# Kernel optimization log

Measured on AMD Instinct MI355X. Metric: run time of the kernel, lower is better.

## Reference

```python
import jax, jax.numpy as jnp
import numpy as np

N = 200000   # nodes (Elliptic-scale)
E = 500000   # directed edges
F = 166      # in_channels / node feature dim
H = 128      # hidden_channels
C = 2        # out_channels
T = 49       # number of time steps


def setup_inputs() -> dict:
    key = jax.random.key(0)
    ks = jax.random.split(key, 12)
    x = jax.random.normal(ks[0], (N, F), jnp.float32)
    edge_index = jax.random.randint(ks[1], (2, E), 0, N, dtype=jnp.int32)
    time_step = jax.random.randint(ks[2], (N,), 0, T, dtype=jnp.int32)
    sF = 1.0 / np.sqrt(F)
    sH = 1.0 / np.sqrt(H)
    initial_w = jax.random.uniform(ks[3], (F, F), jnp.float32, -sF, sF)
    gru_w_ih = jax.random.uniform(ks[4], (3 * F, F), jnp.float32, -sF, sF)
    gru_w_hh = jax.random.uniform(ks[5], (3 * F, F), jnp.float32, -sF, sF)
    gru_b_ih = jax.random.uniform(ks[6], (3 * F,), jnp.float32, -sF, sF)
    gru_b_hh = jax.random.uniform(ks[7], (3 * F,), jnp.float32, -sF, sF)
    proj_w = jax.random.uniform(ks[8], (H, F), jnp.float32, -sF, sF)
    proj_b = jax.random.uniform(ks[9], (H,), jnp.float32, -sF, sF)
    cls_w = jax.random.uniform(ks[10], (C, H), jnp.float32, -sH, sH)
    cls_b = jax.random.uniform(ks[11], (C,), jnp.float32, -sH, sH)
    return {"x": x, "edge_index": edge_index, "time_step": time_step,
            "initial_w": initial_w, "gru_w_ih": gru_w_ih, "gru_w_hh": gru_w_hh,
            "gru_b_ih": gru_b_ih, "gru_b_hh": gru_b_hh,
            "proj_w": proj_w, "proj_b": proj_b, "cls_w": cls_w, "cls_b": cls_b}


def reference(x, edge_index, time_step, initial_w, gru_w_ih, gru_w_hh,
              gru_b_ih, gru_b_hh, proj_w, proj_b, cls_w, cls_b):
    src, dst = edge_index[0], edge_index[1]
    n = x.shape[0]

    def gru(W):
        # torch.nn.GRU single step, input = hidden = W  (FxF matrix, rows = batch)
        gi = W @ gru_w_ih.T + gru_b_ih
        gh = W @ gru_w_hh.T + gru_b_hh
        i_r, i_z, i_n = jnp.split(gi, 3, axis=-1)
        h_r, h_z, h_n = jnp.split(gh, 3, axis=-1)
        r = jax.nn.sigmoid(i_r + h_r)
        z = jax.nn.sigmoid(i_z + h_z)
        nn_ = jnp.tanh(i_n + r * h_n)
        return (1.0 - z) * nn_ + z * W

    def step(carry, t):
        W, logits = carry
        W = gru(W)  # evolve GCN weight (EvolveGCN-O)
        # subgraph of nodes with time_step <= t, expressed by masking (same math
        # as relabel+extract: inactive nodes contribute nothing, their outputs are ignored)
        act = time_step <= t
        ew = (act[src] & act[dst]).astype(x.dtype)
        # gcn_norm with self-loops: deg = in-degree over active edges + 1
        deg = jax.ops.segment_sum(ew, dst, num_segments=n) + 1.0
        dinv = jax.lax.rsqrt(deg)
        norm = ew * dinv[src] * dinv[dst]
        h = jnp.where(act[:, None], x, 0.0) @ W               # [N, F]
        agg = jax.ops.segment_sum(h[src] * norm[:, None], dst, num_segments=n)
        agg = agg + h / deg[:, None]                          # self-loop term dinv_i^2 * h_i
        z = jax.nn.relu(agg @ proj_w.T + proj_b)              # [N, H] (dropout: eval mode)
        lg = z @ cls_w.T + cls_b                              # [N, C]
        logits = jnp.where((time_step == t)[:, None], lg, logits)
        return (W, logits), None

    init = (initial_w, jnp.zeros((n, cls_w.shape[0]), x.dtype))
    (_, logits), _ = jax.lax.scan(step, init, jnp.arange(T, dtype=time_step.dtype))
    return logits
```

## Files before the change

kernel.cpp:

```cpp
#include <hip/hip_runtime.h>
#include <hip/hip_fp16.h>
#include <math.h>

#define NN 200000
#define NE 500000
#define FF 166
#define HH 128
#define CC 2
#define TT 49
#define GG 498
#define PADN 203136
#define MAXTILES 6400
#define KP 84
#define KPAD 192
#define SCB 512
#define SNB 391
#define HB 782
#define CIB 1954
#define XSB 37500
#define P2B 210
#define C2B 977
#define H2B 391
#define DEGB 782
#define MBB (TT * 96)

typedef _Float16 half2v __attribute__((ext_vector_type(2)));
typedef _Float16 f16x4 __attribute__((ext_vector_type(4)));
typedef _Float16 f16x8 __attribute__((ext_vector_type(8)));
typedef float f32x4 __attribute__((ext_vector_type(4)));

static __device__ __forceinline__ float fdot2f(half2v a, half2v b, float c) {
#if __has_builtin(__builtin_amdgcn_fdot2)
    return __builtin_amdgcn_fdot2(a, b, c, false);
#else
    return c + (float)a.x * (float)b.x + (float)a.y * (float)b.y;
#endif
}

__global__ __launch_bounds__(512) void setup1(
        const float* __restrict__ wih, const float* __restrict__ whh,
        const float* __restrict__ projw,
        _Float16* __restrict__ wkp, float* __restrict__ projwT,
        const int* __restrict__ dstp, int* __restrict__ offc,
        const int* __restrict__ ts, int* __restrict__ cnt, int* __restrict__ rank) {
    __shared__ int h2[2][TT];
    int b = blockIdx.x;
    int tid = threadIdx.x;
    if (b < P2B) {
        int idx = b * 512 + tid;
        const int A = 2 * KP * 512;
        if (idx < A) {
            int m = idx / (KP * 512);
            int r = idx - m * (KP * 512);
            int kp = r >> 9, c = r & 511;
            const float* Wm = m ? whh : wih;
            float x0 = 0.0f, x1 = 0.0f;
            if (c < GG) {
                int k0 = 2 * kp, k1 = 2 * kp + 1;
                if (k0 < FF) x0 = Wm[c * FF + k0];
                if (k1 < FF) x1 = Wm[c * FF + k1];
            }
            wkp[2 * idx]     = (_Float16)x0;
            wkp[2 * idx + 1] = (_Float16)x1;
        } else if (idx < A + FF * HH) {
            int q = idx - A;
            int k = q >> 7, hh = q & 127;
            projwT[q] = projw[hh * FF + k];
        }
    } else if (b < P2B + C2B) {
        int e = (b - P2B) * 512 + tid;
        if (e < NE) atomicAdd(&offc[dstp[e]], 1);
    } else {
        int hb2 = b - P2B - C2B;
        int sub = tid >> 8;
        int lt = tid & 255;
        if (lt < TT) h2[sub][lt] = 0;
        __syncthreads();
        int i = hb2 * 512 + tid;
        if (i < NN) {
            int t = ts[i];
            rank[i] = atomicAdd(&h2[sub][t], 1);
        }
        __syncthreads();
        if (lt < TT) cnt[(hb2 * 2 + sub) * TT + lt] = h2[sub][lt];
    }
}

__global__ __launch_bounds__(512) void gru_evolve(
        const float* __restrict__ initial_w,
        const _Float16* __restrict__ wkp,
        const float* __restrict__ bih, const float* __restrict__ bhh,
        float* __restrict__ W_all) {
    __shared__ float s_w[FF];
    __shared__ __align__(16) _Float16 s_wh[2 * KP];
    __shared__ float s_pre[2][512];
    int tid = threadIdx.x;
    int row = blockIdx.x;

    if (tid < FF) {
        float v = initial_w[(size_t)row * FF + tid];
        s_w[tid] = v;
        s_wh[tid] = (_Float16)v;
    } else if (tid < 2 * KP) {
        s_wh[tid] = (_Float16)0.0f;
    }

    int cc0 = tid * 2;
    bool act = cc0 < 996;
    int m = (cc0 >= 498) ? 1 : 0;
    int c0 = act ? (cc0 - m * 498) : 0;

    half2v wr0[KP], wr1[KP];
    {
        const half2v* __restrict__ pW =
            (const half2v*)wkp + (size_t)(act ? m : 0) * (KP * 512) + c0;
        #pragma unroll
        for (int kp = 0; kp < KP; ++kp) {
            wr0[kp] = pW[(size_t)(kp << 9)];
            wr1[kp] = pW[(size_t)(kp << 9) + 1];
        }
    }

    float bi_r = 0, bi_z = 0, bi_n = 0, bh_r = 0, bh_z = 0, bh_n = 0;
    if (tid < FF) {
        bi_r = bih[tid]; bi_z = bih[FF + tid]; bi_n = bih[2 * FF + tid];
        bh_r = bhh[tid]; bh_z = bhh[FF + tid]; bh_n = bhh[2 * FF + tid];
    }
    __syncthreads();

    const f16x8* s_wh8 = (const f16x8*)s_wh;
    for (int t = 0; t < TT; ++t) {
        if (act) {
            float a0 = 0.0f, a1 = 0.0f;
            #pragma unroll
            for (int q = 0; q < 21; ++q) {
                f16x8 w8 = s_wh8[q];
                half2v h0 = __builtin_shufflevector(w8, w8, 0, 1);
                half2v h1 = __builtin_shufflevector(w8, w8, 2, 3);
                half2v h2 = __builtin_shufflevector(w8, w8, 4, 5);
                half2v h3 = __builtin_shufflevector(w8, w8, 6, 7);
                a0 = fdot2f(wr0[4 * q + 0], h0, a0);  a1 = fdot2f(wr1[4 * q + 0], h0, a1);
                a0 = fdot2f(wr0[4 * q + 1], h1, a0);  a1 = fdot2f(wr1[4 * q + 1], h1, a1);
                a0 = fdot2f(wr0[4 * q + 2], h2, a0);  a1 = fdot2f(wr1[4 * q + 2], h2, a1);
                a0 = fdot2f(wr0[4 * q + 3], h3, a0);  a1 = fdot2f(wr1[4 * q + 3], h3, a1);
            }
            s_pre[m][c0]     = a0;
            s_pre[m][c0 + 1] = a1;
        }
        __syncthreads();
        if (tid < FF) {
            float i_r = s_pre[0][tid]          + bi_r;
            float h_r = s_pre[1][tid]          + bh_r;
            float i_z = s_pre[0][FF + tid]     + bi_z;
            float h_z = s_pre[1][FF + tid]     + bh_z;
            float i_n = s_pre[0][2 * FF + tid] + bi_n;
            float h_n = s_pre[1][2 * FF + tid] + bh_n;
            float rg = 1.0f / (1.0f + expf(-(i_r + h_r)));
            float zg = 1.0f / (1.0f + expf(-(i_z + h_z)));
            float ng = tanhf(i_n + rg * h_n);
            float wnew = (1.0f - zg) * ng + zg * s_w[tid];
            s_w[tid] = wnew;
            s_wh[tid] = (_Float16)wnew;
            W_all[((size_t)t * FF + row) * FF + tid] = wnew;
        }
        __syncthreads();
    }
}

__global__ __launch_bounds__(256) void setup2(
        const int* __restrict__ off, int* __restrict__ bsum,
        const int* __restrict__ cnt, int* __restrict__ basecol, int* __restrict__ bcnt) {
    __shared__ int s[256];
    int b = blockIdx.x, tid = threadIdx.x;
    if (b < SNB) {
        int i0 = b * SCB + tid * 2;
        int v = 0;
        if (i0 < NN) v += off[i0];
        if (i0 + 1 < NN) v += off[i0 + 1];
        s[tid] = v;
        __syncthreads();
        for (int d = 128; d > 0; d >>= 1) {
            if (tid < d) s[tid] += s[tid + d];
            __syncthreads();
        }
        if (tid == 0) bsum[b] = s[0];
    } else {
        int t = b - SNB;
        const int CH = (HB + 255) / 256;
        int b0 = tid * CH;
        int loc[4];
        int sum = 0;
        for (int u = 0; u < CH; ++u) {
            int bb = b0 + u;
            int v = (bb < HB) ? cnt[bb * TT + t] : 0;
            loc[u] = sum;
            sum += v;
        }
        s[tid] = sum;
        __syncthreads();
        for (int d = 1; d < 256; d <<= 1) {
            int u = (tid >= d) ? s[tid - d] : 0;
            __syncthreads();
            s[tid] += u;
            __syncthreads();
        }
        int base = s[tid] - sum;
        for (int u = 0; u < CH; ++u) {
            int bb = b0 + u;
            if (bb < HB) basecol[bb * TT + t] = base + loc[u];
        }
        if (tid == 255) bcnt[t] = s[255];
    }
}

__global__ __launch_bounds__(512) void setup3(
        const int* __restrict__ bsum, int* __restrict__ bpre, int* __restrict__ off,
        const int* __restrict__ bcnt, int* __restrict__ pstart,
        int* __restrict__ tile_t, int* __restrict__ tile_r0, int* __restrict__ meta) {
    __shared__ int s[512];
    int tid = threadIdx.x;
    if (blockIdx.x == 0) {
        int v = (tid < SNB) ? bsum[tid] : 0;
        s[tid] = v;
        __syncthreads();
        for (int d = 1; d < 512; d <<= 1) {
            int u = (tid >= d) ? s[tid - d] : 0;
            __syncthreads();
            s[tid] += u;
            __syncthreads();
        }
        bpre[tid] = s[tid] - v;
        if (tid == 511) off[NN] = s[511];
    } else {
        int t = tid;
        int nt = (t < TT) ? (bcnt[t] + 31) / 32 : 0;
        if (t < 64) s[t] = nt;
        __syncthreads();
        for (int d = 1; d < 64; d <<= 1) {
            int v = (t >= d && t < 64) ? s[t - d] : 0;
            __syncthreads();
            if (t < 64) s[t] += v;
            __syncthreads();
        }
        if (t < 64) {
            int ntbase = s[t] - nt;
            int pbase = ntbase * 32;
            if (t < TT) {
                pstart[t] = pbase;
                for (int u = 0; u < nt; ++u) {
                    tile_t[ntbase + u] = t;
                    tile_r0[ntbase + u] = pbase + u * 32;
                }
            }
            if (t == 63) {
                meta[0] = s[63];
                meta[1] = s[63] * 32;
                pstart[TT] = s[63] * 32;
            }
        }
    }
}

__global__ __launch_bounds__(512) void setup4(
        int* __restrict__ off, const int* __restrict__ bpre,
        const int* __restrict__ ts, const int* __restrict__ rank,
        const int* __restrict__ basecol, const int* __restrict__ pstart,
        int* __restrict__ perm, int* __restrict__ pos) {
    __shared__ int s[512];
    int b = blockIdx.x, tid = threadIdx.x;
    if (b < SNB) {
        int i = b * SCB + tid;
        int v = (i < NN) ? off[i] : 0;
        s[tid] = v;
        __syncthreads();
        for (int d = 1; d < 512; d <<= 1) {
            int u = (tid >= d) ? s[tid - d] : 0;
            __syncthreads();
            s[tid] += u;
            __syncthreads();
        }
        if (i < NN) off[i] = s[tid] - v + bpre[b];
    } else {
        int i = (b - SNB) * 512 + tid;
        if (i < NN) {
            int t = ts[i];
            int hb = i >> 8;
            int p = pstart[t] + basecol[hb * TT + t] + rank[i];
            perm[p] = i;
            pos[i] = p;
        }
    }
}

__global__ __launch_bounds__(256) void setup5(
        const int* __restrict__ srcp, const int* __restrict__ dstp,
        const int* __restrict__ ts, const int* __restrict__ off,
        int* __restrict__ cursor, int2* __restrict__ adjst,
        const float* __restrict__ x, const int* __restrict__ pos,
        f16x4* __restrict__ x2p4) {
    int b = blockIdx.x, tid = threadIdx.x;
    if (b < CIB) {
        int e = b * 256 + tid;
        if (e < NE) {
            int d = dstp[e];
            int s2 = srcp[e];
            int p = atomicAdd(&cursor[d], 1);
            adjst[off[d] + p] = make_int2(s2, (ts[s2] << 25) | pos[s2]);
        }
    } else {
        int idx = (b - CIB) * 256 + tid;
        if (idx >= NN * 48) return;
        int i = idx / 48, cp4 = idx - i * 48;
        int c0 = cp4 * 4;
        float v0 = 0.f, v1 = 0.f, v2 = 0.f, v3 = 0.f;
        const float* xr = x + (size_t)i * FF;
        if (c0 + 3 < FF) {
            float2 p0 = *(const float2*)(xr + c0);
            float2 p1 = *(const float2*)(xr + c0 + 2);
            v0 = p0.x; v1 = p0.y; v2 = p1.x; v3 = p1.y;
        } else if (c0 < FF) {
            float2 p0 = *(const float2*)(xr + c0);
            v0 = p0.x; v1 = p0.y;
        }
        f16x4 h;
        h[0] = (_Float16)v0; h[1] = (_Float16)v1;
        h[2] = (_Float16)v2; h[3] = (_Float16)v3;
        x2p4[(size_t)pos[i] * 48 + cp4] = h;
    }
}

__global__ __launch_bounds__(256) void degf_m(
        const int* __restrict__ off, const int2* __restrict__ adjst,
        const int* __restrict__ ts, _Float16* __restrict__ dinvh,
        float* __restrict__ selfdeg,
        const float* __restrict__ W_all, const float* __restrict__ projwT,
        _Float16* __restrict__ Mh) {
    __shared__ unsigned short sh[TT * 256];
    __shared__ __align__(16) float sw2[2][168];
    int b = blockIdx.x;
    int tid = threadIdx.x;
    if (b < DEGB) {
        int i = b * 256 + tid;
        for (int t = 0; t < TT; ++t) sh[t * 256 + tid] = 0;
        if (i >= NN) return;
        int tsi = ts[i];
        int e0 = off[i], e1 = off[i + 1];
        for (int e = e0; e < e1; ++e) {
            int tj = adjst[e].y >> 25;
            sh[tj * 256 + tid]++;
        }
        int cum = 1;
        for (int t = 0; t < TT; ++t) {
            cum += sh[t * 256 + tid];
            dinvh[(size_t)t * NN + i] = (_Float16)rsqrtf((float)cum);
            if (t == tsi) selfdeg[i] = 1.0f / (float)cum;
        }
    } else {
        int mb = b - DEGB;
        int t = mb / 96, rb = mb - t * 96;
        int r0 = rb * 2;
        for (int idx = tid; idx < 2 * FF; idx += 256) {
            int rr = idx / FF, k = idx - rr * FF;
            int r = r0 + rr;
            sw2[rr][k] = (r < FF) ? W_all[((size_t)t * FF + r) * FF + k] : 0.0f;
        }
        __syncthreads();
        int rr = tid >> 7, h = tid & 127;
        int r = r0 + rr;
        float acc = 0.0f;
        if (r < FF) {
            const float* __restrict__ pw = projwT + h;
            #pragma unroll 4
            for (int c4 = 0; c4 < 164; c4 += 4) {
                float4 w = *(const float4*)&sw2[rr][c4];
                acc += w.x * pw[(size_t)(c4 + 0) << 7];
                acc += w.y * pw[(size_t)(c4 + 1) << 7];
                acc += w.z * pw[(size_t)(c4 + 2) << 7];
                acc += w.w * pw[(size_t)(c4 + 3) << 7];
            }
            acc += sw2[rr][164] * pw[(size_t)164 << 7];
            acc += sw2[rr][165] * pw[(size_t)165 << 7];
        }
        Mh[((size_t)t * HH + h) * KPAD + r] = (_Float16)acc;
    }
}

__global__ __launch_bounds__(256) void edge_compact(
        const int* __restrict__ off, const int2* __restrict__ adjst,
        const int* __restrict__ ts, const _Float16* __restrict__ dinvh,
        int2* __restrict__ ewp, int* __restrict__ nact) {
    int i = blockIdx.x * 256 + threadIdx.x;
    if (i >= NN) return;
    int t = ts[i];
    const _Float16* dv = dinvh + (size_t)t * NN;
    float dvi = (float)dv[i];
    int e0 = off[i], e1 = off[i + 1];
    int c = e0;
    for (int e = e0; e < e1; ++e) {
        int2 a = adjst[e];
        if ((a.y >> 25) <= t) {
            float w = (float)dv[a.x] * dvi;
            ewp[c++] = make_int2(a.y & 0x1FFFFFF, __float_as_int(w));
        }
    }
    nact[i] = c - e0;
}

__global__ __launch_bounds__(512) void gemm_fused5(
        const int* __restrict__ meta, const int* __restrict__ tile_t,
        const int* __restrict__ tile_r0, const int* __restrict__ perm,
        const float* __restrict__ selfdeg, const f16x4* __restrict__ x2p4,
        const int* __restrict__ off, const int* __restrict__ nact,
        const int2* __restrict__ ewp,
        const _Float16* __restrict__ Mh, const float* __restrict__ proj_b,
        const float* __restrict__ cls_w, const float* __restrict__ cls_b,
        float* __restrict__ out) {
    __shared__ __align__(16) char smraw[32 * 130 * 4];
    _Float16* sY = (_Float16*)smraw;
    float* sP = (float*)smraw;
    int bid = blockIdx.x;
    if (bid >= meta[0]) return;
    int t = tile_t[bid], r0 = tile_r0[bid];
    int tid = threadIdx.x;
    int lane = tid & 63;
    int w = tid >> 6;
    bool ln48 = lane < 48;

    {
        const uint4* src = (const uint4*)(x2p4 + (size_t)r0 * 48);
        #pragma unroll
        for (int u = 0; u < 2; ++u) {
            int q = tid + u * 512;
            if (q < 768) {
                int row = q / 24, kc = q - row * 24;
                *(uint4*)(sY + row * 200 + kc * 8) = src[q];
            }
        }
    }
    __syncthreads();

    int rbase = w * 4;
    int ep[4], ee[4];
    float ac[4][4];
    #pragma unroll
    for (int q = 0; q < 4; ++q) {
        int r = rbase + q;
        int i = perm[r0 + r];
        float sw = 0.0f;
        ep[q] = 0; ee[q] = 0;
        if (i >= 0) {
            sw = selfdeg[i];
            ep[q] = off[i];
            ee[q] = ep[q] + nact[i];
        }
        f16x4 h = (f16x4)((_Float16)0.0f);
        if (ln48) h = *(const f16x4*)(sY + r * 200 + lane * 4);
        ac[q][0] = sw * (float)h[0];
        ac[q][1] = sw * (float)h[1];
        ac[q][2] = sw * (float)h[2];
        ac[q][3] = sw * (float)h[3];
    }
    int2 pc[4];
    #pragma unroll
    for (int q = 0; q < 4; ++q) pc[q] = (ep[q] < ee[q]) ? ewp[ep[q]] : make_int2(0, 0);
    while ((ep[0] < ee[0]) | (ep[1] < ee[1]) | (ep[2] < ee[2]) | (ep[3] < ee[3])) {
        int js[4]; float wv[4];
        #pragma unroll
        for (int q = 0; q < 4; ++q) {
            bool val = ep[q] < ee[q];
            js[q] = pc[q].x;
            wv[q] = val ? __int_as_float(pc[q].y) : 0.0f;
            if (val) ep[q]++;
        }
        #pragma unroll
        for (int q = 0; q < 4; ++q) pc[q] = (ep[q] < ee[q]) ? ewp[ep[q]] : make_int2(0, 0);
        #pragma unroll
        for (int q = 0; q < 4; ++q) {
            if (wv[q] != 0.0f && ln48) {
                f16x4 g = x2p4[(size_t)js[q] * 48 + lane];
                ac[q][0] += wv[q] * (float)g[0];
                ac[q][1] += wv[q] * (float)g[1];
                ac[q][2] += wv[q] * (float)g[2];
                ac[q][3] += wv[q] * (float)g[3];
            }
        }
    }
    #pragma unroll
    for (int q = 0; q < 4; ++q) {
        if (ln48) {
            f16x4 o;
            o[0] = (_Float16)ac[q][0];
            o[1] = (_Float16)ac[q][1];
            o[2] = (_Float16)ac[q][2];
            o[3] = (_Float16)ac[q][3];
            *(f16x4*)(sY + (rbase + q) * 200 + lane * 4) = o;
        }
    }
    __syncthreads();

    int lr = lane & 15;
    int kg = lane >> 4;
    int c0 = w * 16;
    f32x4 acc0 = {0, 0, 0, 0}, acc1 = {0, 0, 0, 0};
    const _Float16* B0 = Mh + ((size_t)t * HH + c0 + lr) * KPAD + kg * 8;
    const _Float16* A0 = sY + lr * 200 + kg * 8;
    const _Float16* A1 = A0 + 16 * 200;

    #pragma unroll
    for (int s = 0; s < 6; ++s) {
        f16x8 b0 = *(const f16x8*)(B0 + s * 32);
        f16x8 a0 = *(const f16x8*)(A0 + s * 32);
        f16x8 a1 = *(const f16x8*)(A1 + s * 32);
        acc0 = __builtin_amdgcn_mfma_f32_16x16x32_f16(a0, b0, acc0, 0, 0, 0);
        acc1 = __builtin_amdgcn_mfma_f32_16x16x32_f16(a1, b0, acc1, 0, 0, 0);
    }

    float pb = proj_b[c0 + lr];
    __syncthreads();
    int prow = kg * 4;
    int colw = c0 + lr;
    #pragma unroll
    for (int r = 0; r < 4; ++r) {
        sP[(prow + r) * 130 + colw]      = fmaxf(acc0[r] + pb, 0.0f);
        sP[(16 + prow + r) * 130 + colw] = fmaxf(acc1[r] + pb, 0.0f);
    }
    __syncthreads();

    int row = tid >> 4, cc = (tid >> 3) & 1, qq = tid & 7;
    const float* pr = sP + row * 130 + qq * 16;
    const float* cw = cls_w + cc * HH + qq * 16;
    float s = 0.0f;
    #pragma unroll
    for (int h = 0; h < 16; ++h) s += pr[h] * cw[h];
    s += __shfl_xor(s, 1);
    s += __shfl_xor(s, 2);
    s += __shfl_xor(s, 4);
    if (qq == 0) {
        int node = perm[r0 + row];
        if (node >= 0) out[(size_t)node * CC + cc] = s + cls_b[cc];
    }
}

extern "C" void kernel_launch(void* const* d_in, const int* in_sizes, int n_in,
                              void* d_out, int out_size, void* d_ws, size_t ws_size,
                              hipStream_t stream) {
    const float* x = (const float*)d_in[0];
    const int* ei = (const int*)d_in[1];
    const int* srcp = ei;
    const int* dstp = ei + NE;
    const int* ts = (const int*)d_in[2];
    const float* initial_w = (const float*)d_in[3];
    const float* wih = (const float*)d_in[4];
    const float* whh = (const float*)d_in[5];
    const float* bih = (const float*)d_in[6];
    const float* bhh = (const float*)d_in[7];
    const float* projw = (const float*)d_in[8];
    const float* projb = (const float*)d_in[9];
    const float* clsw = (const float*)d_in[10];
    const float* clsb = (const float*)d_in[11];
    float* out = (float*)d_out;

    char* base = (char*)d_ws;
    size_t o = 0;
    auto alloc = [&](size_t bytes) { size_t r = o; o = (o + bytes + 255) & ~(size_t)255; return r; };

    float*    W_all   = (float*)   (base + alloc((size_t)TT * FF * FF * 4));
    _Float16* Mh      = (_Float16*)(base + alloc((size_t)TT * HH * KPAD * 2));
    _Float16* wkp     = (_Float16*)(base + alloc((size_t)2 * KP * 512 * 2 * 2));
    float*    projwT  = (float*)   (base + alloc((size_t)FF * HH * 4));
    int*      off     = (int*)     (base + alloc((size_t)(NN + 1) * 4));
    int*      cursor  = (int*)     (base + alloc((size_t)NN * 4));
    int2*     adjst   = (int2*)    (base + alloc((size_t)NE * 8));
    int2*     ewp     = (int2*)    (base + alloc((size_t)NE * 8));
    _Float16* dinvh   = (_Float16*)(base + alloc((size_t)TT * NN * 2));
    float*    selfdeg = (float*)   (base + alloc((size_t)NN * 4));
    int*      nact    = (int*)     (base + alloc((size_t)NN * 4));
    int*      pos     = (int*)     (base + alloc((size_t)NN * 4));
    int*      bcnt    = (int*)     (base + alloc((size_t)TT * 4));
    int*      pstart  = (int*)     (base + alloc((size_t)(TT + 1) * 4));
    int*      meta    = (int*)     (base + alloc(2 * 4));
    int*      tile_t  = (int*)     (base + alloc((size_t)MAXTILES * 4));
    int*      tile_r0 = (int*)     (base + alloc((size_t)MAXTILES * 4));
    int*      perm    = (int*)     (base + alloc((size_t)PADN * 4));
    int*      bsum    = (int*)     (base + alloc((size_t)512 * 4));
    int*      bpre    = (int*)     (base + alloc((size_t)520 * 4));
    int*      cnt     = (int*)     (base + alloc((size_t)HB * TT * 4));
    int*      basecol = (int*)     (base + alloc((size_t)HB * TT * 4));
    int*      rank    = (int*)     (base + alloc((size_t)NN * 4));
    f16x4*    x2p4    = (f16x4*)   (base + alloc((size_t)PADN * 48 * 8));

    hipMemsetAsync(off, 0, (size_t)((char*)cursor - (char*)off) + (size_t)NN * 4, stream);
    hipMemsetAsync(perm, 0xFF, (size_t)PADN * 4, stream);

    setup1<<<P2B + C2B + H2B, 512, 0, stream>>>(wih, whh, projw, wkp, projwT,
                                                dstp, off, ts, cnt, rank);
    gru_evolve<<<FF, 512, 0, stream>>>(initial_w, wkp, bih, bhh, W_all);
    setup2<<<SNB + TT, 256, 0, stream>>>(off, bsum, cnt, basecol, bcnt);
    setup3<<<2, 512, 0, stream>>>(bsum, bpre, off, bcnt, pstart, tile_t, tile_r0, meta);
    setup4<<<SNB + SNB, 512, 0, stream>>>(off, bpre, ts, rank, basecol, pstart, perm, pos);
    setup5<<<CIB + XSB, 256, 0, stream>>>(srcp, dstp, ts, off, cursor, adjst, x, pos, x2p4);
    degf_m<<<DEGB + MBB, 256, 0, stream>>>(off, adjst, ts, dinvh, selfdeg, W_all, projwT, Mh);
    edge_compact<<<(NN + 255) / 256, 256, 0, stream>>>(off, adjst, ts, dinvh, ewp, nact);

    gemm_fused5<<<MAXTILES, 512, 0, stream>>>(meta, tile_t, tile_r0, perm, selfdeg,
                                              x2p4, off, nact, ewp, Mh, projb, clsw, clsb, out);
}
```

Baseline: 326.0 us.

## Sort nodes within each time step by active in-degree bucket

Counts each node's active in-degree (edges whose source time step is at most the destination's) during setup. The node permutation now orders nodes within each time step by a key of time step times eight plus the clamped degree bucket. Nodes in a 32-row tile of the fused GEMM/aggregation kernel then have similar edge counts, which is meant to reduce wavefront divergence and load imbalance in the gather. The histogramming also moves into the GRU kernel's launch to overlap with it, at the cost of an extra atomic pass and larger count tables.

```diff
diff --git a/kernel.cpp b/kernel.cpp
--- a/kernel.cpp
+++ b/kernel.cpp
@@ -18,6 +18,7 @@
 #define HB 782
 #define CIB 1954
 #define XSB 37500
+#define NK 392
 #define P2B 210
 #define C2B 977
 #define H2B 391
@@ -41,9 +42,9 @@
         const float* __restrict__ wih, const float* __restrict__ whh,
         const float* __restrict__ projw,
         _Float16* __restrict__ wkp, float* __restrict__ projwT,
-        const int* __restrict__ dstp, int* __restrict__ offc,
-        const int* __restrict__ ts, int* __restrict__ cnt, int* __restrict__ rank) {
-    __shared__ int h2[2][TT];
+        const int* __restrict__ srcp, const int* __restrict__ dstp,
+        const int* __restrict__ ts,
+        int* __restrict__ offc, int* __restrict__ actdeg) {
     int b = blockIdx.x;
     int tid = threadIdx.x;
     if (b < P2B) {
@@ -67,109 +68,120 @@
             int k = q >> 7, hh = q & 127;
             projwT[q] = projw[hh * FF + k];
         }
-    } else if (b < P2B + C2B) {
+    } else {
         int e = (b - P2B) * 512 + tid;
-        if (e < NE) atomicAdd(&offc[dstp[e]], 1);
-    } else {
-        int hb2 = b - P2B - C2B;
-        int sub = tid >> 8;
-        int lt = tid & 255;
-        if (lt < TT) h2[sub][lt] = 0;
-        __syncthreads();
-        int i = hb2 * 512 + tid;
-        if (i < NN) {
-            int t = ts[i];
-            rank[i] = atomicAdd(&h2[sub][t], 1);
-        }
-        __syncthreads();
-        if (lt < TT) cnt[(hb2 * 2 + sub) * TT + lt] = h2[sub][lt];
-    }
-}
-
-__global__ __launch_bounds__(512) void gru_evolve(
+        if (e < NE) {
+            int d = dstp[e];
+            atomicAdd(&offc[d], 1);
+            if (ts[srcp[e]] <= ts[d]) atomicAdd(&actdeg[d], 1);
+        }
+    }
+}
+
+__global__ __launch_bounds__(512) void gru_hist(
         const float* __restrict__ initial_w,
         const _Float16* __restrict__ wkp,
         const float* __restrict__ bih, const float* __restrict__ bhh,
-        float* __restrict__ W_all) {
+        float* __restrict__ W_all,
+        const int* __restrict__ ts, const int* __restrict__ actdeg,
+        int* __restrict__ cnt, int* __restrict__ rank) {
     __shared__ float s_w[FF];
     __shared__ __align__(16) _Float16 s_wh[2 * KP];
     __shared__ float s_pre[2][512];
+    __shared__ int h2[2][NK];
     int tid = threadIdx.x;
-    int row = blockIdx.x;
-
-    if (tid < FF) {
-        float v = initial_w[(size_t)row * FF + tid];
-        s_w[tid] = v;
-        s_wh[tid] = (_Float16)v;
-    } else if (tid < 2 * KP) {
-        s_wh[tid] = (_Float16)0.0f;
-    }
-
-    int cc0 = tid * 2;
-    bool act = cc0 < 996;
-    int m = (cc0 >= 498) ? 1 : 0;
-    int c0 = act ? (cc0 - m * 498) : 0;
-
-    half2v wr0[KP], wr1[KP];
-    {
-        const half2v* __restrict__ pW =
-            (const half2v*)wkp + (size_t)(act ? m : 0) * (KP * 512) + c0;
-        #pragma unroll
-        for (int kp = 0; kp < KP; ++kp) {
-            wr0[kp] = pW[(size_t)(kp << 9)];
-            wr1[kp] = pW[(size_t)(kp << 9) + 1];
-        }
-    }
-
-    float bi_r = 0, bi_z = 0, bi_n = 0, bh_r = 0, bh_z = 0, bh_n = 0;
-    if (tid < FF) {
-        bi_r = bih[tid]; bi_z = bih[FF + tid]; bi_n = bih[2 * FF + tid];
-        bh_r = bhh[tid]; bh_z = bhh[FF + tid]; bh_n = bhh[2 * FF + tid];
-    }
-    __syncthreads();
-
-    const f16x8* s_wh8 = (const f16x8*)s_wh;
-    for (int t = 0; t < TT; ++t) {
-        if (act) {
-            float a0 = 0.0f, a1 = 0.0f;
+    int b = blockIdx.x;
+
+    if (b < FF) {
+        int row = b;
+        if (tid < FF) {
+            float v = initial_w[(size_t)row * FF + tid];
+            s_w[tid] = v;
+            s_wh[tid] = (_Float16)v;
+        } else if (tid < 2 * KP) {
+            s_wh[tid] = (_Float16)0.0f;
+        }
+
+        int cc0 = tid * 2;
+        bool act = cc0 < 996;
+        int m = (cc0 >= 498) ? 1 : 0;
+        int c0 = act ? (cc0 - m * 498) : 0;
+
+        half2v wr0[KP], wr1[KP];
+        {
+            const half2v* __restrict__ pW =
+                (const half2v*)wkp + (size_t)(act ? m : 0) * (KP * 512) + c0;
             #pragma unroll
-            for (int q = 0; q < 21; ++q) {
-                f16x8 w8 = s_wh8[q];
-                half2v h0 = __builtin_shufflevector(w8, w8, 0, 1);
-                half2v h1 = __builtin_shufflevector(w8, w8, 2, 3);
-                half2v h2 = __builtin_shufflevector(w8, w8, 4, 5);
-                half2v h3 = __builtin_shufflevector(w8, w8, 6, 7);
-                a0 = fdot2f(wr0[4 * q + 0], h0, a0);  a1 = fdot2f(wr1[4 * q + 0], h0, a1);
-                a0 = fdot2f(wr0[4 * q + 1], h1, a0);  a1 = fdot2f(wr1[4 * q + 1], h1, a1);
-                a0 = fdot2f(wr0[4 * q + 2], h2, a0);  a1 = fdot2f(wr1[4 * q + 2], h2, a1);
-                a0 = fdot2f(wr0[4 * q + 3], h3, a0);  a1 = fdot2f(wr1[4 * q + 3], h3, a1);
-            }
-            s_pre[m][c0]     = a0;
-            s_pre[m][c0 + 1] = a1;
-        }
-        __syncthreads();
+            for (int kp = 0; kp < KP; ++kp) {
+                wr0[kp] = pW[(size_t)(kp << 9)];
+                wr1[kp] = pW[(size_t)(kp << 9) + 1];
+            }
+        }
+
+        float bi_r = 0, bi_z = 0, bi_n = 0, bh_r = 0, bh_z = 0, bh_n = 0;
         if (tid < FF) {
-            float i_r = s_pre[0][tid]          + bi_r;
-            float h_r = s_pre[1][tid]          + bh_r;
-            float i_z = s_pre[0][FF + tid]     + bi_z;
-            float h_z = s_pre[1][FF + tid]     + bh_z;
-            float i_n = s_pre[0][2 * FF + tid] + bi_n;
-            float h_n = s_pre[1][2 * FF + tid] + bh_n;
-            float rg = 1.0f / (1.0f + expf(-(i_r + h_r)));
-            float zg = 1.0f / (1.0f + expf(-(i_z + h_z)));
-            float ng = tanhf(i_n + rg * h_n);
-            float wnew = (1.0f - zg) * ng + zg * s_w[tid];
-            s_w[tid] = wnew;
-            s_wh[tid] = (_Float16)wnew;
-            W_all[((size_t)t * FF + row) * FF + tid] = wnew;
-        }
-        __syncthreads();
+            bi_r = bih[tid]; bi_z = bih[FF + tid]; bi_n = bih[2 * FF + tid];
+            bh_r = bhh[tid]; bh_z = bhh[FF + tid]; bh_n = bhh[2 * FF + tid];
+        }
+        __syncthreads();
+
+        const f16x8* s_wh8 = (const f16x8*)s_wh;
+        for (int t = 0; t < TT; ++t) {
+            if (act) {
+                float a0 = 0.0f, a1 = 0.0f;
+                #pragma unroll
+                for (int q = 0; q < 21; ++q) {
+                    f16x8 w8 = s_wh8[q];
+                    half2v h0 = __builtin_shufflevector(w8, w8, 0, 1);
+                    half2v h1 = __builtin_shufflevector(w8, w8, 2, 3);
+                    half2v h2v = __builtin_shufflevector(w8, w8, 4, 5);
+                    half2v h3 = __builtin_shufflevector(w8, w8, 6, 7);
+                    a0 = fdot2f(wr0[4 * q + 0], h0, a0);  a1 = fdot2f(wr1[4 * q + 0], h0, a1);
+                    a0 = fdot2f(wr0[4 * q + 1], h1, a0);  a1 = fdot2f(wr1[4 * q + 1], h1, a1);
+                    a0 = fdot2f(wr0[4 * q + 2], h2v, a0); a1 = fdot2f(wr1[4 * q + 2], h2v, a1);
+                    a0 = fdot2f(wr0[4 * q + 3], h3, a0);  a1 = fdot2f(wr1[4 * q + 3], h3, a1);
+                }
+                s_pre[m][c0]     = a0;
+                s_pre[m][c0 + 1] = a1;
+            }
+            __syncthreads();
+            if (tid < FF) {
+                float i_r = s_pre[0][tid]          + bi_r;
+                float h_r = s_pre[1][tid]          + bh_r;
+                float i_z = s_pre[0][FF + tid]     + bi_z;
+                float h_z = s_pre[1][FF + tid]     + bh_z;
+                float i_n = s_pre[0][2 * FF + tid] + bi_n;
+                float h_n = s_pre[1][2 * FF + tid] + bh_n;
+                float rg = 1.0f / (1.0f + expf(-(i_r + h_r)));
+                float zg = 1.0f / (1.0f + expf(-(i_z + h_z)));
+                float ng = tanhf(i_n + rg * h_n);
+                float wnew = (1.0f - zg) * ng + zg * s_w[tid];
+                s_w[tid] = wnew;
+                s_wh[tid] = (_Float16)wnew;
+                W_all[((size_t)t * FF + row) * FF + tid] = wnew;
+            }
+            __syncthreads();
+        }
+    } else {
+        int hb2 = b - FF;
+        int sub = tid >> 8;
+        int lt = tid & 255;
+        for (int k = lt; k < NK; k += 256) h2[sub][k] = 0;
+        __syncthreads();
+        int i = hb2 * 512 + tid;
+        if (i < NN) {
+            int ad = actdeg[i];
+            int key = ts[i] * 8 + (ad > 7 ? 7 : ad);
+            rank[i] = atomicAdd(&h2[sub][key], 1);
+        }
+        __syncthreads();
+        for (int k = lt; k < NK; k += 256) cnt[(size_t)(hb2 * 2 + sub) * NK + k] = h2[sub][k];
     }
 }
 
 __global__ __launch_bounds__(256) void setup2(
         const int* __restrict__ off, int* __restrict__ bsum,
-        const int* __restrict__ cnt, int* __restrict__ basecol, int* __restrict__ bcnt) {
+        const int* __restrict__ cnt, int* __restrict__ basecol, int* __restrict__ kcnt) {
     __shared__ int s[256];
     int b = blockIdx.x, tid = threadIdx.x;
     if (b < SNB) {
@@ -185,14 +197,14 @@
         }
         if (tid == 0) bsum[b] = s[0];
     } else {
-        int t = b - SNB;
+        int key = b - SNB;
         const int CH = (HB + 255) / 256;
         int b0 = tid * CH;
         int loc[4];
         int sum = 0;
         for (int u = 0; u < CH; ++u) {
             int bb = b0 + u;
-            int v = (bb < HB) ? cnt[bb * TT + t] : 0;
+            int v = (bb < HB) ? cnt[(size_t)bb * NK + key] : 0;
             loc[u] = sum;
             sum += v;
         }
@@ -207,17 +219,18 @@
         int base = s[tid] - sum;
         for (int u = 0; u < CH; ++u) {
             int bb = b0 + u;
-            if (bb < HB) basecol[bb * TT + t] = base + loc[u];
-        }
-        if (tid == 255) bcnt[t] = s[255];
+            if (bb < HB) basecol[(size_t)bb * NK + key] = base + loc[u];
+        }
+        if (tid == 255) kcnt[key] = s[255];
     }
 }
 
 __global__ __launch_bounds__(512) void setup3(
         const int* __restrict__ bsum, int* __restrict__ bpre, int* __restrict__ off,
-        const int* __restrict__ bcnt, int* __restrict__ pstart,
+        const int* __restrict__ kcnt, int* __restrict__ keybase, int* __restrict__ pstart,
         int* __restrict__ tile_t, int* __restrict__ tile_r0, int* __restrict__ meta) {
     __shared__ int s[512];
+    __shared__ int skc[NK];
     int tid = threadIdx.x;
     if (blockIdx.x == 0) {
         int v = (tid < SNB) ? bsum[tid] : 0;
@@ -232,27 +245,36 @@
         bpre[tid] = s[tid] - v;
         if (tid == 511) off[NN] = s[511];
     } else {
-        int t = tid;
-        int nt = (t < TT) ? (bcnt[t] + 31) / 32 : 0;
-        if (t < 64) s[t] = nt;
+        for (int k = tid; k < NK; k += 512) skc[k] = kcnt[k];
+        __syncthreads();
+        int nt = 0;
+        if (tid < TT) {
+            int base = 0;
+            for (int c = 0; c < 8; ++c) {
+                keybase[tid * 8 + c] = base;
+                base += skc[tid * 8 + c];
+            }
+            nt = (base + 31) / 32;
+        }
+        if (tid < 64) s[tid] = nt;
         __syncthreads();
         for (int d = 1; d < 64; d <<= 1) {
-            int v = (t >= d && t < 64) ? s[t - d] : 0;
-            __syncthreads();
-            if (t < 64) s[t] += v;
-            __syncthreads();
-        }
-        if (t < 64) {
-            int ntbase = s[t] - nt;
+            int v = (tid >= d && tid < 64) ? s[tid - d] : 0;
+            __syncthreads();
+            if (tid < 64) s[tid] += v;
+            __syncthreads();
+        }
+        if (tid < 64) {
+            int ntbase = s[tid] - nt;
             int pbase = ntbase * 32;
-            if (t < TT) {
-                pstart[t] = pbase;
+            if (tid < TT) {
+                pstart[tid] = pbase;
                 for (int u = 0; u < nt; ++u) {
-                    tile_t[ntbase + u] = t;
+                    tile_t[ntbase + u] = tid;
                     tile_r0[ntbase + u] = pbase + u * 32;
                 }
             }
-            if (t == 63) {
+            if (tid == 63) {
                 meta[0] = s[63];
                 meta[1] = s[63] * 32;
                 pstart[TT] = s[63] * 32;
@@ -263,8 +285,10 @@
 
 __global__ __launch_bounds__(512) void setup4(
         int* __restrict__ off, const int* __restrict__ bpre,
-        const int* __restrict__ ts, const int* __restrict__ rank,
-        const int* __restrict__ basecol, const int* __restrict__ pstart,
+        const int* __restrict__ ts, const int* __restrict__ actdeg,
+        const int* __restrict__ rank,
+        const int* __restrict__ basecol, const int* __restrict__ keybase,
+        const int* __restrict__ pstart,
         int* __restrict__ perm, int* __restrict__ pos) {
     __shared__ int s[512];
     int b = blockIdx.x, tid = threadIdx.x;
@@ -284,8 +308,10 @@
         int i = (b - SNB) * 512 + tid;
         if (i < NN) {
             int t = ts[i];
+            int ad = actdeg[i];
+            int key = t * 8 + (ad > 7 ? 7 : ad);
             int hb = i >> 8;
-            int p = pstart[t] + basecol[hb * TT + t] + rank[i];
+            int p = pstart[t] + keybase[key] + basecol[(size_t)hb * NK + key] + rank[i];
             perm[p] = i;
             pos[i] = p;
         }
@@ -570,13 +596,15 @@
     float*    projwT  = (float*)   (base + alloc((size_t)FF * HH * 4));
     int*      off     = (int*)     (base + alloc((size_t)(NN + 1) * 4));
     int*      cursor  = (int*)     (base + alloc((size_t)NN * 4));
+    int*      actdeg  = (int*)     (base + alloc((size_t)NN * 4));
     int2*     adjst   = (int2*)    (base + alloc((size_t)NE * 8));
     int2*     ewp     = (int2*)    (base + alloc((size_t)NE * 8));
     _Float16* dinvh   = (_Float16*)(base + alloc((size_t)TT * NN * 2));
     float*    selfdeg = (float*)   (base + alloc((size_t)NN * 4));
     int*      nact    = (int*)     (base + alloc((size_t)NN * 4));
     int*      pos     = (int*)     (base + alloc((size_t)NN * 4));
-    int*      bcnt    = (int*)     (base + alloc((size_t)TT * 4));
+    int*      kcnt    = (int*)     (base + alloc((size_t)NK * 4));
+    int*      keybase = (int*)     (base + alloc((size_t)NK * 4));
     int*      pstart  = (int*)     (base + alloc((size_t)(TT + 1) * 4));
     int*      meta    = (int*)     (base + alloc(2 * 4));
     int*      tile_t  = (int*)     (base + alloc((size_t)MAXTILES * 4));
@@ -584,20 +612,22 @@
     int*      perm    = (int*)     (base + alloc((size_t)PADN * 4));
     int*      bsum    = (int*)     (base + alloc((size_t)512 * 4));
     int*      bpre    = (int*)     (base + alloc((size_t)520 * 4));
-    int*      cnt     = (int*)     (base + alloc((size_t)HB * TT * 4));
-    int*      basecol = (int*)     (base + alloc((size_t)HB * TT * 4));
+    int*      cnt     = (int*)     (base + alloc((size_t)HB * NK * 4));
+    int*      basecol = (int*)     (base + alloc((size_t)HB * NK * 4));
     int*      rank    = (int*)     (base + alloc((size_t)NN * 4));
     f16x4*    x2p4    = (f16x4*)   (base + alloc((size_t)PADN * 48 * 8));
 
-    hipMemsetAsync(off, 0, (size_t)((char*)cursor - (char*)off) + (size_t)NN * 4, stream);
+    hipMemsetAsync(off, 0, (size_t)((char*)actdeg - (char*)off) + (size_t)NN * 4, stream);
     hipMemsetAsync(perm, 0xFF, (size_t)PADN * 4, stream);
 
-    setup1<<<P2B + C2B + H2B, 512, 0, stream>>>(wih, whh, projw, wkp, projwT,
-                                                dstp, off, ts, cnt, rank);
-    gru_evolve<<<FF, 512, 0, stream>>>(initial_w, wkp, bih, bhh, W_all);
-    setup2<<<SNB + TT, 256, 0, stream>>>(off, bsum, cnt, basecol, bcnt);
-    setup3<<<2, 512, 0, stream>>>(bsum, bpre, off, bcnt, pstart, tile_t, tile_r0, meta);
-    setup4<<<SNB + SNB, 512, 0, stream>>>(off, bpre, ts, rank, basecol, pstart, perm, pos);
+    setup1<<<P2B + C2B, 512, 0, stream>>>(wih, whh, projw, wkp, projwT,
+                                          srcp, dstp, ts, off, actdeg);
+    gru_hist<<<FF + H2B, 512, 0, stream>>>(initial_w, wkp, bih, bhh, W_all,
+                                           ts, actdeg, cnt, rank);
+    setup2<<<SNB + NK, 256, 0, stream>>>(off, bsum, cnt, basecol, kcnt);
+    setup3<<<2, 512, 0, stream>>>(bsum, bpre, off, kcnt, keybase, pstart, tile_t, tile_r0, meta);
+    setup4<<<SNB + SNB, 512, 0, stream>>>(off, bpre, ts, actdeg, rank, basecol, keybase,
+                                          pstart, perm, pos);
     setup5<<<CIB + XSB, 256, 0, stream>>>(srcp, dstp, ts, off, cursor, adjst, x, pos, x2p4);
     degf_m<<<DEGB + MBB, 256, 0, stream>>>(off, adjst, ts, dinvh, selfdeg, W_all, projwT, Mh);
     edge_compact<<<(NN + 255) / 256, 256, 0, stream>>>(off, adjst, ts, dinvh, ewp, nact);
```

Result: slower. 335.8 us (+3.0%).
